# Kernel tuning notes

Hardware: AMD Instinct MI355X
Metric: run time of the kernel (lower is better)

## Reference

```python
import jax, jax.numpy as jnp
import numpy as np

N_NODES = 50000
N_EDGES = 800000
D_IN = 64
F1 = 64
F2 = 64
D_HID = 100


def setup_inputs() -> dict:
    key = jax.random.key(0)
    ks = jax.random.split(key, 12)
    x = jax.random.normal(ks[0], (N_NODES, D_IN), dtype=jnp.float32)
    edge_src = jax.random.randint(ks[1], (N_EDGES,), 0, N_NODES, dtype=jnp.int32)
    edge_dst = jax.random.randint(ks[2], (N_EDGES,), 0, N_NODES, dtype=jnp.int32)
    # stands in for pre-normalized GCN adjacency values (D^-1/2 (A+I) D^-1/2)
    edge_weight = jax.random.uniform(ks[3], (N_EDGES,), dtype=jnp.float32)
    def glorot(k, shape):
        lim = np.sqrt(6.0 / (shape[0] + shape[1]))
        return jax.random.uniform(k, shape, jnp.float32, -lim, lim)
    W1 = glorot(ks[4], (D_IN, F1))
    b1 = jnp.zeros((F1,), jnp.float32)
    W2 = glorot(ks[5], (F1, F2))
    b2 = jnp.zeros((F2,), jnp.float32)
    Wd = glorot(ks[6], (F2, D_HID))
    bd = jnp.zeros((D_HID,), jnp.float32)
    Wo = glorot(ks[7], (D_HID, 1))
    bo = jnp.zeros((1,), jnp.float32)
    return {"x": x, "edge_src": edge_src, "edge_dst": edge_dst,
            "edge_weight": edge_weight, "W1": W1, "b1": b1, "W2": W2,
            "b2": b2, "Wd": Wd, "bd": bd, "Wo": Wo, "bo": bo}


def _gcn_conv(x, edge_src, edge_dst, edge_weight, W, b):
    # spektral GCNConv: out = swish(A_norm @ (X @ W) + b)
    h = x @ W                                        # [N, F]
    msg = h[edge_src] * edge_weight[:, None]          # [E, F] gather + scale
    agg = jax.ops.segment_sum(msg, edge_dst, num_segments=N_NODES)  # [N, F]
    return jax.nn.swish(agg + b)


def reference(x, edge_src, edge_dst, edge_weight, W1, b1, W2, b2, Wd, bd, Wo, bo):
    h = _gcn_conv(x, edge_src, edge_dst, edge_weight, W1, b1)
    h = _gcn_conv(h, edge_src, edge_dst, edge_weight, W2, b2)
    h = jax.nn.swish(h @ Wd + bd)                    # Dense(100, swish)
    return jax.nn.sigmoid(h @ Wo + bo)               # Dense(1, sigmoid) -> [N, 1]
```

## Files before the change

kernel.cpp:

```cpp
#include <hip/hip_runtime.h>
#include <hip/hip_fp16.h>

#define N_NODES 50000
#define N_EDGES 800000
#define D 64
#define DHID 100
#define NTILES (N_NODES / 16)
#define NCT 7
#define CAP 64
#define NGROUPS 4
#define NSLICES 780
#define FILL_BLOCKS (NGROUPS * NSLICES)
#define MM_BLOCKS ((NTILES + 3) / 4)
#define DST_PER_GROUP (N_NODES / NGROUPS)

typedef unsigned short ushort;
typedef unsigned int uint;
typedef __attribute__((ext_vector_type(8))) short s16x8;
typedef __attribute__((ext_vector_type(4))) float f32x4;

#define MFMA16(A, B, C) __builtin_amdgcn_mfma_f32_16x16x32_bf16((A), (B), (C), 0, 0, 0)

__device__ __forceinline__ float swishf(float x) { return x / (1.0f + __expf(-x)); }

__device__ __forceinline__ ushort f2bf(float f) {
    uint u = __float_as_uint(f);
    uint r = (u + 0x7fffu + ((u >> 16) & 1u)) >> 16;
    return (ushort)r;
}
__device__ __forceinline__ float bf2f(ushort h) { return __uint_as_float((uint)h << 16); }
__device__ __forceinline__ float bf_lo(uint d) { return __uint_as_float(d << 16); }
__device__ __forceinline__ float bf_hi(uint d) { return __uint_as_float(d & 0xffff0000u); }

__device__ __forceinline__ float hwf(uint e) {
    return __half2float(__ushort_as_half((ushort)(e >> 16)));
}

__device__ __forceinline__ void accum8(float* acc, uint4 v, float w) {
    acc[0] = fmaf(w, bf_lo(v.x), acc[0]);
    acc[1] = fmaf(w, bf_hi(v.x), acc[1]);
    acc[2] = fmaf(w, bf_lo(v.y), acc[2]);
    acc[3] = fmaf(w, bf_hi(v.y), acc[3]);
    acc[4] = fmaf(w, bf_lo(v.z), acc[4]);
    acc[5] = fmaf(w, bf_hi(v.z), acc[5]);
    acc[6] = fmaf(w, bf_lo(v.w), acc[6]);
    acc[7] = fmaf(w, bf_hi(v.w), acc[7]);
}

__device__ __forceinline__ void gather_node(const ushort* __restrict__ H,
                                            const uint* __restrict__ bucket,
                                            int degv, int j, int fg, float* acc) {
#pragma unroll
    for (int t = 0; t < 8; ++t) acc[t] = 0.f;
    for (int base = 0; base < degv; base += 32) {
        int s0 = base + j * 4;
        uint4 e = *((const uint4*)(bucket + s0));
        float w0 = (s0 + 0 < degv) ? hwf(e.x) : 0.f;
        float w1 = (s0 + 1 < degv) ? hwf(e.y) : 0.f;
        float w2 = (s0 + 2 < degv) ? hwf(e.z) : 0.f;
        float w3 = (s0 + 3 < degv) ? hwf(e.w) : 0.f;
        uint s0i = min(e.x & 0xffffu, (uint)(N_NODES - 1));
        uint s1i = min(e.y & 0xffffu, (uint)(N_NODES - 1));
        uint s2i = min(e.z & 0xffffu, (uint)(N_NODES - 1));
        uint s3i = min(e.w & 0xffffu, (uint)(N_NODES - 1));
        uint4 v0 = *((const uint4*)(H + ((size_t)s0i << 6) + (fg << 3)));
        uint4 v1 = *((const uint4*)(H + ((size_t)s1i << 6) + (fg << 3)));
        uint4 v2 = *((const uint4*)(H + ((size_t)s2i << 6) + (fg << 3)));
        uint4 v3 = *((const uint4*)(H + ((size_t)s3i << 6) + (fg << 3)));
        accum8(acc, v0, w0);
        accum8(acc, v1, w1);
        accum8(acc, v2, w2);
        accum8(acc, v3, w3);
    }
#pragma unroll
    for (int t = 0; t < 8; ++t) {
        acc[t] += __shfl_xor(acc[t], 8, 64);
        acc[t] += __shfl_xor(acc[t], 16, 64);
        acc[t] += __shfl_xor(acc[t], 32, 64);
    }
}

__global__ __launch_bounds__(256) void fill_and_l1(const int* __restrict__ src,
                                                   const int* __restrict__ dst,
                                                   const float* __restrict__ w,
                                                   int* __restrict__ deg,
                                                   uint* __restrict__ csr,
                                                   const float* __restrict__ X,
                                                   const float* __restrict__ W,
                                                   const float* __restrict__ W2,
                                                   const float* __restrict__ Wd,
                                                   short* __restrict__ W2T2,
                                                   short* __restrict__ WdT2,
                                                   ushort* __restrict__ H) {
    __shared__ __align__(16) short sBT[2][D][72];
    int tid = threadIdx.x;

    if (blockIdx.x < FILL_BLOCKS) {
        const int g = blockIdx.x & (NGROUPS - 1);
        const int s = blockIdx.x >> 2;
        const int lo = g * DST_PER_GROUP;
        const int hi = lo + DST_PER_GROUP;
        for (int e = s * 256 + tid; e < N_EDGES; e += NSLICES * 256) {
            int d = dst[e];
            if (d >= lo && d < hi) {
                uint hw = (uint)__half_as_ushort(__float2half_rn(w[e]));
                uint payload = (uint)src[e] | (hw << 16);
                int r = atomicAdd(&deg[d], 1);
                r = min(r, CAP - 1);
                csr[(d << 6) + r] = payload;
            }
        }
        return;
    }

    if (blockIdx.x >= FILL_BLOCKS + MM_BLOCKS) {
        if (blockIdx.x == FILL_BLOCKS + MM_BLOCKS) {
            for (int idx = tid; idx < D * D; idx += 256) {
                int k = idx >> 6, c = idx & 63;
                float wv = W2[idx];
                ushort hi = f2bf(wv);
                W2T2[(size_t)c * D + k] = (short)hi;
                W2T2[(size_t)(D + c) * D + k] = (short)f2bf(wv - bf2f(hi));
            }
        } else {
            for (int idx = tid; idx < NCT * 16 * D; idx += 256) {
                int jj = idx >> 6, k = idx & 63;
                float wv = (jj < DHID) ? Wd[k * DHID + jj] : 0.f;
                ushort hi = f2bf(wv);
                WdT2[(size_t)jj * D + k] = (short)hi;
                WdT2[(size_t)(NCT * 16 + jj) * D + k] = (short)f2bf(wv - bf2f(hi));
            }
        }
        return;
    }

    for (int idx = tid; idx < D * D; idx += 256) {
        int k = idx >> 6, c = idx & 63;
        float wv = W[idx];
        ushort hi = f2bf(wv);
        sBT[0][c][k] = (short)hi;
        sBT[1][c][k] = (short)f2bf(wv - bf2f(hi));
    }
    __syncthreads();
    int wv_ = tid >> 6, lane = tid & 63, quad = lane >> 4, m = lane & 15;
    int tile = min((blockIdx.x - FILL_BLOCKS) * 4 + wv_, NTILES - 1);
    int node0 = tile * 16;

    f32x4 acc[4] = {{0,0,0,0},{0,0,0,0},{0,0,0,0},{0,0,0,0}};
#pragma unroll
    for (int kt = 0; kt < 2; ++kt) {
        int k0 = kt * 32 + quad * 8;
        const float* xp = X + ((size_t)(node0 + m) << 6) + k0;
        float4 xa = *((const float4*)xp);
        float4 xb = *((const float4*)(xp + 4));
        float xv[8] = {xa.x, xa.y, xa.z, xa.w, xb.x, xb.y, xb.z, xb.w};
        s16x8 ahi, alo;
#pragma unroll
        for (int jj = 0; jj < 8; ++jj) {
            ushort hi = f2bf(xv[jj]);
            ahi[jj] = (short)hi;
            alo[jj] = (short)f2bf(xv[jj] - bf2f(hi));
        }
#pragma unroll
        for (int ct = 0; ct < 4; ++ct) {
            int n = ct * 16 + m;
            s16x8 bhi = *((const s16x8*)&sBT[0][n][k0]);
            s16x8 blo = *((const s16x8*)&sBT[1][n][k0]);
            acc[ct] = MFMA16(ahi, bhi, acc[ct]);
            acc[ct] = MFMA16(ahi, blo, acc[ct]);
            acc[ct] = MFMA16(alo, bhi, acc[ct]);
        }
    }
    __syncthreads();
    short (*rep)[16][72] = (short(*)[16][72])&sBT[0][0][0];
#pragma unroll
    for (int ct = 0; ct < 4; ++ct)
#pragma unroll
        for (int r = 0; r < 4; ++r)
            rep[wv_][quad * 4 + r][ct * 16 + m] = (short)f2bf(acc[ct][r]);
#pragma unroll
    for (int half = 0; half < 2; ++half) {
        int r = (lane >> 3) + half * 8;
        int c0 = (lane & 7) * 8;
        s16x8 v = *((const s16x8*)&rep[wv_][r][c0]);
        *((s16x8*)(H + ((size_t)(node0 + r) << 6) + c0)) = v;
    }
}

__global__ __launch_bounds__(256) void gather_act(const ushort* __restrict__ H,
                                                  const int* __restrict__ deg,
                                                  const uint* __restrict__ csr,
                                                  const float* __restrict__ bias,
                                                  ushort* __restrict__ actOut) {
    int tid = threadIdx.x;
    int wave = tid >> 6, lane = tid & 63;
    int j = lane >> 3, fg = lane & 7;
    int node = blockIdx.x * 4 + wave;
    int degv = min(deg[node], CAP);
    const uint* bucket = csr + ((size_t)node << 6);

    float acc[8];
    gather_node(H, bucket, degv, j, fg, acc);
    if (j == 0) {
        float4 ba = ((const float4*)bias)[fg * 2];
        float4 bb = ((const float4*)bias)[fg * 2 + 1];
        float r0 = swishf(acc[0] + ba.x);
        float r1 = swishf(acc[1] + ba.y);
        float r2 = swishf(acc[2] + ba.z);
        float r3 = swishf(acc[3] + ba.w);
        float r4 = swishf(acc[4] + bb.x);
        float r5 = swishf(acc[5] + bb.y);
        float r6 = swishf(acc[6] + bb.z);
        float r7 = swishf(acc[7] + bb.w);
        uint4 u;
        u.x = (uint)f2bf(r0) | ((uint)f2bf(r1) << 16);
        u.y = (uint)f2bf(r2) | ((uint)f2bf(r3) << 16);
        u.z = (uint)f2bf(r4) | ((uint)f2bf(r5) << 16);
        u.w = (uint)f2bf(r6) | ((uint)f2bf(r7) << 16);
        *((uint4*)(actOut + ((size_t)node << 6) + (fg << 3))) = u;
    }
}

__global__ __launch_bounds__(256) void gather_tail(const ushort* __restrict__ act1,
                                                   const int* __restrict__ deg,
                                                   const uint* __restrict__ csr,
                                                   const short* __restrict__ W2T2,
                                                   const float* __restrict__ b2,
                                                   const short* __restrict__ WdT2,
                                                   const float* __restrict__ bd,
                                                   const float* __restrict__ Wo,
                                                   const float* __restrict__ bo,
                                                   float* __restrict__ out) {
    __shared__ __align__(16) float sAgg[16][72];
    __shared__ __align__(16) short sAct2[16][72];
    __shared__ float sPart[4][16];
    int tid = threadIdx.x;
    int wv = tid >> 6, lane = tid & 63;
    int j = lane >> 3, fg = lane & 7;
    int quad = lane >> 4, m = lane & 15;
    int node0 = blockIdx.x * 16;

    for (int t = 0; t < 4; ++t) {
        int nl = wv * 4 + t;
        int node = node0 + nl;
        int degv = min(deg[node], CAP);
        const uint* bucket = csr + ((size_t)node << 6);
        float acc[8];
        gather_node(act1, bucket, degv, j, fg, acc);
        if (j == 0) {
            float4 u0 = {acc[0], acc[1], acc[2], acc[3]};
            float4 u1 = {acc[4], acc[5], acc[6], acc[7]};
            *((float4*)&sAgg[nl][fg * 8]) = u0;
            *((float4*)&sAgg[nl][fg * 8 + 4]) = u1;
        }
    }
    __syncthreads();

    {
        f32x4 acc = {0, 0, 0, 0};
        int n = wv * 16 + m;
#pragma unroll
        for (int kt = 0; kt < 2; ++kt) {
            int k0 = kt * 32 + quad * 8;
            float4 xa = *((const float4*)&sAgg[m][k0]);
            float4 xb = *((const float4*)&sAgg[m][k0 + 4]);
            float xv[8] = {xa.x, xa.y, xa.z, xa.w, xb.x, xb.y, xb.z, xb.w};
            s16x8 ahi, alo;
#pragma unroll
            for (int jj = 0; jj < 8; ++jj) {
                ushort hi = f2bf(xv[jj]);
                ahi[jj] = (short)hi;
                alo[jj] = (short)f2bf(xv[jj] - bf2f(hi));
            }
            s16x8 bhi = *((const s16x8*)(W2T2 + (size_t)n * D + k0));
            s16x8 blo = *((const s16x8*)(W2T2 + (size_t)(D + n) * D + k0));
            acc = MFMA16(ahi, bhi, acc);
            acc = MFMA16(ahi, blo, acc);
            acc = MFMA16(alo, bhi, acc);
        }
        float bv = b2[n];
#pragma unroll
        for (int r = 0; r < 4; ++r)
            sAct2[quad * 4 + r][n] = (short)f2bf(swishf(acc[r] + bv));
    }
    __syncthreads();

    float part[4] = {0, 0, 0, 0};
#pragma unroll
    for (int cc = 0; cc < 2; ++cc) {
        int ct = wv + cc * 4;
        if (ct < NCT) {
            f32x4 acc = {0, 0, 0, 0};
            int n = ct * 16 + m;
#pragma unroll
            for (int kt = 0; kt < 2; ++kt) {
                int k0 = kt * 32 + quad * 8;
                s16x8 a = *((const s16x8*)&sAct2[m][k0]);
                s16x8 bhi = *((const s16x8*)(WdT2 + (size_t)n * D + k0));
                s16x8 blo = *((const s16x8*)(WdT2 + (size_t)(NCT * 16 + n) * D + k0));
                acc = MFMA16(a, bhi, acc);
                acc = MFMA16(a, blo, acc);
            }
            float bdv = (n < DHID) ? bd[n] : 0.f;
            float wov = (n < DHID) ? Wo[n] : 0.f;
#pragma unroll
            for (int r = 0; r < 4; ++r)
                part[r] = fmaf(swishf(acc[r] + bdv), wov, part[r]);
        }
    }
#pragma unroll
    for (int r = 0; r < 4; ++r) {
        part[r] += __shfl_xor(part[r], 1, 64);
        part[r] += __shfl_xor(part[r], 2, 64);
        part[r] += __shfl_xor(part[r], 4, 64);
        part[r] += __shfl_xor(part[r], 8, 64);
    }
    if (m == 0) {
#pragma unroll
        for (int r = 0; r < 4; ++r)
            sPart[wv][quad * 4 + r] = part[r];
    }
    __syncthreads();
    if (tid < 16) {
        float z = sPart[0][tid] + sPart[1][tid] + sPart[2][tid] + sPart[3][tid] + bo[0];
        out[node0 + tid] = 1.f / (1.f + __expf(-z));
    }
}

extern "C" void kernel_launch(void* const* d_in, const int* in_sizes, int n_in,
                              void* d_out, int out_size, void* d_ws, size_t ws_size,
                              hipStream_t stream) {
    const float* x   = (const float*)d_in[0];
    const int* esrc  = (const int*)d_in[1];
    const int* edst  = (const int*)d_in[2];
    const float* ew  = (const float*)d_in[3];
    const float* W1  = (const float*)d_in[4];
    const float* b1  = (const float*)d_in[5];
    const float* W2  = (const float*)d_in[6];
    const float* b2  = (const float*)d_in[7];
    const float* Wd  = (const float*)d_in[8];
    const float* bd  = (const float*)d_in[9];
    const float* Wo  = (const float*)d_in[10];
    const float* bo  = (const float*)d_in[11];
    float* out = (float*)d_out;

    char* ws = (char*)d_ws;
    ushort* H1   = (ushort*)ws;  ws += (size_t)N_NODES * D * sizeof(ushort);
    ushort* act1 = (ushort*)ws;  ws += (size_t)N_NODES * D * sizeof(ushort);
    uint* csr    = (uint*)ws;    ws += (size_t)N_NODES * CAP * sizeof(uint);
    int* deg     = (int*)ws;     ws += (size_t)N_NODES * sizeof(int);
    short* W2T2  = (short*)ws;   ws += (size_t)2 * D * D * sizeof(short);
    short* WdT2  = (short*)ws;   ws += (size_t)2 * NCT * 16 * D * sizeof(short);

    const int gBlocks = N_NODES / 4;

    hipMemsetAsync(deg, 0, (size_t)N_NODES * sizeof(int), stream);

    fill_and_l1<<<FILL_BLOCKS + MM_BLOCKS + 2, 256, 0, stream>>>(
        esrc, edst, ew, deg, csr, x, W1, W2, Wd, W2T2, WdT2, H1);

    gather_act<<<gBlocks, 256, 0, stream>>>(H1, deg, csr, b1, act1);

    gather_tail<<<NTILES, 256, 0, stream>>>(act1, deg, csr, W2T2, b2, WdT2, bd, Wo, bo, out);
}
```

Baseline: 187.6 us.

## Process two nodes per wavefront in gathers and use nontemporal streaming loads

Each 64-lane wavefront in the gather kernels now handles two destination nodes with 32 lanes each: 4 edge slots by 8 feature groups per node instead of 8 by 8. The cross-lane reduction drops a shuffle stage and a guard skips edge chunks beyond the node's degree. With average degree 16, fewer lanes sit idle on padded slots. The edge-list and X loads in the fill/L1 kernel also switch to nontemporal loads so they do not pollute the cache. The trade-off is more loop iterations per lane for high-degree nodes and fewer gather blocks.

Measured after the change: 181.0 us. -3.5%, faster.

```diff
diff --git a/kernel.cpp b/kernel.cpp
--- a/kernel.cpp
+++ b/kernel.cpp
@@ -47,36 +47,37 @@
     acc[7] = fmaf(w, bf_hi(v.w), acc[7]);
 }
 
-__device__ __forceinline__ void gather_node(const ushort* __restrict__ H,
-                                            const uint* __restrict__ bucket,
-                                            int degv, int j, int fg, float* acc) {
+__device__ __forceinline__ void gather_node2(const ushort* __restrict__ H,
+                                             const uint* __restrict__ bucket,
+                                             int degv, int j, int fg, float* acc) {
 #pragma unroll
     for (int t = 0; t < 8; ++t) acc[t] = 0.f;
-    for (int base = 0; base < degv; base += 32) {
+    for (int base = 0; base < degv; base += 16) {
         int s0 = base + j * 4;
-        uint4 e = *((const uint4*)(bucket + s0));
-        float w0 = (s0 + 0 < degv) ? hwf(e.x) : 0.f;
-        float w1 = (s0 + 1 < degv) ? hwf(e.y) : 0.f;
-        float w2 = (s0 + 2 < degv) ? hwf(e.z) : 0.f;
-        float w3 = (s0 + 3 < degv) ? hwf(e.w) : 0.f;
-        uint s0i = min(e.x & 0xffffu, (uint)(N_NODES - 1));
-        uint s1i = min(e.y & 0xffffu, (uint)(N_NODES - 1));
-        uint s2i = min(e.z & 0xffffu, (uint)(N_NODES - 1));
-        uint s3i = min(e.w & 0xffffu, (uint)(N_NODES - 1));
-        uint4 v0 = *((const uint4*)(H + ((size_t)s0i << 6) + (fg << 3)));
-        uint4 v1 = *((const uint4*)(H + ((size_t)s1i << 6) + (fg << 3)));
-        uint4 v2 = *((const uint4*)(H + ((size_t)s2i << 6) + (fg << 3)));
-        uint4 v3 = *((const uint4*)(H + ((size_t)s3i << 6) + (fg << 3)));
-        accum8(acc, v0, w0);
-        accum8(acc, v1, w1);
-        accum8(acc, v2, w2);
-        accum8(acc, v3, w3);
+        if (s0 < degv) {
+            uint4 e = *((const uint4*)(bucket + s0));
+            float w0 = hwf(e.x);
+            float w1 = (s0 + 1 < degv) ? hwf(e.y) : 0.f;
+            float w2 = (s0 + 2 < degv) ? hwf(e.z) : 0.f;
+            float w3 = (s0 + 3 < degv) ? hwf(e.w) : 0.f;
+            uint s0i = min(e.x & 0xffffu, (uint)(N_NODES - 1));
+            uint s1i = min(e.y & 0xffffu, (uint)(N_NODES - 1));
+            uint s2i = min(e.z & 0xffffu, (uint)(N_NODES - 1));
+            uint s3i = min(e.w & 0xffffu, (uint)(N_NODES - 1));
+            uint4 v0 = *((const uint4*)(H + ((size_t)s0i << 6) + (fg << 3)));
+            uint4 v1 = *((const uint4*)(H + ((size_t)s1i << 6) + (fg << 3)));
+            uint4 v2 = *((const uint4*)(H + ((size_t)s2i << 6) + (fg << 3)));
+            uint4 v3 = *((const uint4*)(H + ((size_t)s3i << 6) + (fg << 3)));
+            accum8(acc, v0, w0);
+            accum8(acc, v1, w1);
+            accum8(acc, v2, w2);
+            accum8(acc, v3, w3);
+        }
     }
 #pragma unroll
     for (int t = 0; t < 8; ++t) {
         acc[t] += __shfl_xor(acc[t], 8, 64);
         acc[t] += __shfl_xor(acc[t], 16, 64);
-        acc[t] += __shfl_xor(acc[t], 32, 64);
     }
 }
 
@@ -101,10 +102,12 @@
         const int lo = g * DST_PER_GROUP;
         const int hi = lo + DST_PER_GROUP;
         for (int e = s * 256 + tid; e < N_EDGES; e += NSLICES * 256) {
-            int d = dst[e];
+            int d = __builtin_nontemporal_load(dst + e);
             if (d >= lo && d < hi) {
-                uint hw = (uint)__half_as_ushort(__float2half_rn(w[e]));
-                uint payload = (uint)src[e] | (hw << 16);
+                float wval = __builtin_nontemporal_load(w + e);
+                int sval = __builtin_nontemporal_load(src + e);
+                uint hw = (uint)__half_as_ushort(__float2half_rn(wval));
+                uint payload = (uint)sval | (hw << 16);
                 int r = atomicAdd(&deg[d], 1);
                 r = min(r, CAP - 1);
                 csr[(d << 6) + r] = payload;
@@ -151,9 +154,9 @@
     for (int kt = 0; kt < 2; ++kt) {
         int k0 = kt * 32 + quad * 8;
         const float* xp = X + ((size_t)(node0 + m) << 6) + k0;
-        float4 xa = *((const float4*)xp);
-        float4 xb = *((const float4*)(xp + 4));
-        float xv[8] = {xa.x, xa.y, xa.z, xa.w, xb.x, xb.y, xb.z, xb.w};
+        f32x4 xa = __builtin_nontemporal_load((const f32x4*)xp);
+        f32x4 xb = __builtin_nontemporal_load((const f32x4*)(xp + 4));
+        float xv[8] = {xa[0], xa[1], xa[2], xa[3], xb[0], xb[1], xb[2], xb[3]};
         s16x8 ahi, alo;
 #pragma unroll
         for (int jj = 0; jj < 8; ++jj) {
@@ -194,13 +197,13 @@
                                                   ushort* __restrict__ actOut) {
     int tid = threadIdx.x;
     int wave = tid >> 6, lane = tid & 63;
-    int j = lane >> 3, fg = lane & 7;
-    int node = blockIdx.x * 4 + wave;
+    int h = lane >> 5, j = (lane >> 3) & 3, fg = lane & 7;
+    int node = blockIdx.x * 8 + wave * 2 + h;
     int degv = min(deg[node], CAP);
     const uint* bucket = csr + ((size_t)node << 6);
 
     float acc[8];
-    gather_node(H, bucket, degv, j, fg, acc);
+    gather_node2(H, bucket, degv, j, fg, acc);
     if (j == 0) {
         float4 ba = ((const float4*)bias)[fg * 2];
         float4 bb = ((const float4*)bias)[fg * 2 + 1];
@@ -236,17 +239,17 @@
     __shared__ float sPart[4][16];
     int tid = threadIdx.x;
     int wv = tid >> 6, lane = tid & 63;
-    int j = lane >> 3, fg = lane & 7;
+    int h = lane >> 5, j = (lane >> 3) & 3, fg = lane & 7;
     int quad = lane >> 4, m = lane & 15;
     int node0 = blockIdx.x * 16;
 
-    for (int t = 0; t < 4; ++t) {
-        int nl = wv * 4 + t;
+    for (int t = 0; t < 2; ++t) {
+        int nl = wv * 4 + t * 2 + h;
         int node = node0 + nl;
         int degv = min(deg[node], CAP);
         const uint* bucket = csr + ((size_t)node << 6);
         float acc[8];
-        gather_node(act1, bucket, degv, j, fg, acc);
+        gather_node2(act1, bucket, degv, j, fg, acc);
         if (j == 0) {
             float4 u0 = {acc[0], acc[1], acc[2], acc[3]};
             float4 u1 = {acc[4], acc[5], acc[6], acc[7]};
@@ -352,7 +355,7 @@
     short* W2T2  = (short*)ws;   ws += (size_t)2 * D * D * sizeof(short);
     short* WdT2  = (short*)ws;   ws += (size_t)2 * NCT * 16 * D * sizeof(short);
 
-    const int gBlocks = N_NODES / 4;
+    const int gBlocks = N_NODES / 8;
 
     hipMemsetAsync(deg, 0, (size_t)N_NODES * sizeof(int), stream);
 
```
